# Kernel optimization log

Measured on AMD Instinct MI355X. Metric: run time of the kernel, lower is better.

Reference implementation:

```python
import jax, jax.numpy as jnp
import numpy as np

N = 2048
C = 1024
B = 4
LN_EPS = 1e-5
SCALE = 1.0 / np.sqrt(N)  # module uses 1/sqrt(n), not 1/sqrt(d)


def setup_inputs() -> dict:
    key = jax.random.key(0)
    ks = jax.random.split(key, 4)
    x = jax.random.normal(ks[0], (B, C, N), dtype=jnp.float32)
    position = jax.random.normal(ks[1], (N, N), dtype=jnp.float32)
    ln_gamma = jnp.ones((C,), dtype=jnp.float32)
    ln_beta = jnp.zeros((C,), dtype=jnp.float32)
    W_qkv = jax.random.normal(ks[2], (3 * C, C), dtype=jnp.float32) / np.sqrt(C)
    b_qkv = jnp.zeros((3 * C,), dtype=jnp.float32)
    return {"x": x, "position": position, "ln_gamma": ln_gamma,
            "ln_beta": ln_beta, "W_qkv": W_qkv, "b_qkv": b_qkv}


def reference(x, position, ln_gamma, ln_beta, W_qkv, b_qkv):
    # x: [B, C, N] -> tokens-last layout; permute to [B, N, C]
    h = jnp.transpose(x, (0, 2, 1))
    # LayerNorm over channel dim
    mu = jnp.mean(h, axis=-1, keepdims=True)
    var = jnp.mean(jnp.square(h - mu), axis=-1, keepdims=True)
    h = (h - mu) * jax.lax.rsqrt(var + LN_EPS) * ln_gamma + ln_beta
    # QKV projection: torch Linear -> h @ W^T + b
    qkv = jnp.einsum('bnc,dc->bnd', h, W_qkv) + b_qkv
    q, k, v = jnp.split(qkv, 3, axis=-1)  # each [B, N, C]
    # scores: [B, N, N] with learned additive position bias
    scores = jnp.einsum('bic,bjc->bij', q, k) * SCALE + position
    attn = jax.nn.softmax(scores, axis=-1)
    out = jnp.einsum('bij,bjc->bic', attn, v)  # [B, N, C]
    return jnp.transpose(out, (0, 2, 1))  # [B, C, N]
```

## Files before the change

### kernel.cpp

```cpp
#include <hip/hip_runtime.h>
#include <stdint.h>

typedef unsigned short u16;
typedef unsigned int u32;

#define NTOK 2048
#define CDIM 1024
#define BSZ  4
#define MTOT (BSZ * NTOK)
#define QKVD 3072
#define SM_SCALE 0.02209708691207961f
#define INV_SM_SCALE 45.254833995939045f

typedef __bf16 bf16x8 __attribute__((ext_vector_type(8)));
typedef float f32x4 __attribute__((ext_vector_type(4)));

__device__ __forceinline__ u16 f2bf(float f) {
  u32 u = __float_as_uint(f);
  u += 0x7fffu + ((u >> 16) & 1u);
  return (u16)(u >> 16);
}

__global__ __launch_bounds__(256) void wconv_kernel(const float* __restrict__ W,
                                                    u16* __restrict__ Wb, int n8,
                                                    float* __restrict__ RS) {
  int i = blockIdx.x * 256 + threadIdx.x;
  if (i < MTOT) RS[i] = 0.f;
  if (i >= n8) return;
  const float4* p = (const float4*)W + (size_t)i * 2;
  float4 a = p[0], b = p[1];
  uint4 o;
  o.x = (u32)f2bf(a.x) | ((u32)f2bf(a.y) << 16);
  o.y = (u32)f2bf(a.z) | ((u32)f2bf(a.w) << 16);
  o.z = (u32)f2bf(b.x) | ((u32)f2bf(b.y) << 16);
  o.w = (u32)f2bf(b.z) | ((u32)f2bf(b.w) << 16);
  ((uint4*)Wb)[i] = o;
}

__global__ __launch_bounds__(512) void ln_kernel(const float* __restrict__ x,
                                                 const float* __restrict__ gamma,
                                                 const float* __restrict__ beta,
                                                 u16* __restrict__ h) {
  int blk = blockIdx.x;
  int b = blk >> 6;
  int n0 = (blk & 63) << 5;
  int t = threadIdx.x;
  int nl = t & 31;
  int cp = t >> 5;
  const float* xb = x + (size_t)b * CDIM * NTOK + n0 + nl;

  float v[64];
  float s = 0.f, ss = 0.f;
#pragma unroll
  for (int k = 0; k < 64; ++k) {
    v[k] = xb[(size_t)(cp + (k << 4)) * NTOK];
    s += v[k]; ss += v[k] * v[k];
  }
  __shared__ float ps[16][32], pss[16][32];
  __shared__ float mean_s[32], rstd_s[32];
  ps[cp][nl] = s; pss[cp][nl] = ss;
  __syncthreads();
  if (t < 32) {
    float m = 0.f, q = 0.f;
#pragma unroll
    for (int p = 0; p < 16; ++p) { m += ps[p][t]; q += pss[p][t]; }
    float mu = m * (1.f / CDIM);
    float var = q * (1.f / CDIM) - mu * mu;
    mean_s[t] = mu;
    rstd_s[t] = rsqrtf(var + 1e-5f);
  }
  __syncthreads();
  float mu_n = mean_s[nl], rs_n = rstd_s[nl];

  __shared__ float tile[64][33];
  int tn = t >> 4, cl = t & 15;
#pragma unroll
  for (int kk = 0; kk < 16; ++kk) {
    __syncthreads();
#pragma unroll
    for (int i = 0; i < 4; ++i) {
      int c = (kk << 6) + (i << 4) + cp;
      tile[(i << 4) + cp][nl] = (v[(kk << 2) + i] - mu_n) * rs_n * gamma[c] + beta[c];
    }
    __syncthreads();
    uint2 pk;
    pk.x = (u32)f2bf(tile[(cl << 2) + 0][tn]) | ((u32)f2bf(tile[(cl << 2) + 1][tn]) << 16);
    pk.y = (u32)f2bf(tile[(cl << 2) + 2][tn]) | ((u32)f2bf(tile[(cl << 2) + 3][tn]) << 16);
    *(uint2*)&h[(size_t)(b * NTOK + n0 + tn) * CDIM + (kk << 6) + (cl << 2)] = pk;
  }
}

__device__ __forceinline__ void gld_lds16(const void* g, void* l) {
  __builtin_amdgcn_global_load_lds(
      (const __attribute__((address_space(1))) void*)g,
      (__attribute__((address_space(3))) void*)l, 16, 0, 0);
}

__device__ __forceinline__ void stage128(const char* g, long ld, char* lds, int t) {
  const long rb = (long)(t >> 2) * ld + ((((t & 3) - (t >> 3)) & 3) << 4);
#pragma unroll
  for (int i = 0; i < 2; ++i)
    gld_lds16(g + rb + (long)(i * 64) * ld,
              lds + ((t >> 6) << 10) + (i << 12));
}

template <int EPI>
__global__ __launch_bounds__(256, 3) void gemm_kernel(
    const u16* __restrict__ A, int lda, long sA,
    const u16* __restrict__ B, int ldb, long sB, int K,
    const float* __restrict__ bias,
    const float* __restrict__ pos,
    u16* __restrict__ Cb, int ldc, long sC,
    u16* __restrict__ KD,
    u16* __restrict__ VT,
    float* __restrict__ CT, long sCT,
    float* __restrict__ RS)
{
  __shared__ char smem[32768];

  const int GX = gridDim.x, GY = gridDim.y;
  const int hb = ((int)blockIdx.z * GY + blockIdx.y) * GX + blockIdx.x;
  const int MX = GX >> 3;
  const int k8 = hb & 7, j8 = hb >> 3;
  const int m = k8 * MX + (j8 % MX);
  const int rest = j8 / MX;
  const int n = rest % GY;
  const int bz = rest / GY;

  A += (size_t)bz * sA;
  B += (size_t)bz * sB;
  const int bm0 = m * 128;
  const int bn0 = n * 128;

  const int t = threadIdx.x;
  const int wave = t >> 6;
  const int wm = wave >> 1, wn = wave & 1;
  const int MROW = wm * 64, NCOL = wn * 64;
  const int lr = t & 15, lk = (t & 63) >> 4;
  const int fragoff = lr * 64 + (((lk + (lr >> 1)) & 3) << 4);

  const long lda2 = (long)lda * 2, ldb2 = (long)ldb * 2;
  const char* Agb = (const char*)A + (size_t)bm0 * lda2;
  const char* Bgb = (const char*)B + (size_t)bn0 * ldb2;

  f32x4 acc[4][4];
  if (EPI == 1) {
#pragma unroll
    for (int mm = 0; mm < 4; ++mm) {
      const int row = bm0 + MROW + mm * 16 + (lk << 2);
#pragma unroll
      for (int nn = 0; nn < 4; ++nn) {
        const int col = bn0 + NCOL + nn * 16 + lr;
#pragma unroll
        for (int r = 0; r < 4; ++r)
          acc[mm][nn][r] = pos[(size_t)(row + r) * NTOK + col] * INV_SM_SCALE;
      }
    }
  } else {
#pragma unroll
    for (int mm = 0; mm < 4; ++mm)
#pragma unroll
      for (int nn = 0; nn < 4; ++nn) acc[mm][nn] = (f32x4){0.f, 0.f, 0.f, 0.f};
  }

  const int nt = K >> 6;
  for (int kt = 0; kt < nt; ++kt) {
    __syncthreads();
    const long kb = (long)kt * 128;
    stage128(Agb + kb,      lda2, smem,          t);
    stage128(Agb + kb + 64, lda2, smem + 8192,   t);
    stage128(Bgb + kb,      ldb2, smem + 16384,  t);
    stage128(Bgb + kb + 64, ldb2, smem + 24576,  t);
    __syncthreads();

#pragma unroll
    for (int ks = 0; ks < 2; ++ks) {
      const char* Ab = smem + ks * 8192;
      const char* Bb = smem + 16384 + ks * 8192;
      bf16x8 av[4], bv[4];
#pragma unroll
      for (int i = 0; i < 4; ++i)
        av[i] = *(const bf16x8*)(Ab + (MROW + i * 16) * 64 + fragoff);
#pragma unroll
      for (int i = 0; i < 4; ++i)
        bv[i] = *(const bf16x8*)(Bb + (NCOL + i * 16) * 64 + fragoff);
#pragma unroll
      for (int mm = 0; mm < 4; ++mm)
#pragma unroll
        for (int nn = 0; nn < 4; ++nn)
          acc[mm][nn] = __builtin_amdgcn_mfma_f32_16x16x32_bf16(av[mm], bv[nn],
                                                                acc[mm][nn], 0, 0, 0);
    }
  }

#pragma unroll
  for (int mm = 0; mm < 4; ++mm) {
    const int row = bm0 + MROW + mm * 16 + (lk << 2);
    float rs[4] = {0.f, 0.f, 0.f, 0.f};
    float inv[4];
    if (EPI == 2) {
      const float4 rsv = *(const float4*)(RS + (size_t)bz * NTOK + row);
      inv[0] = 1.f / rsv.x; inv[1] = 1.f / rsv.y;
      inv[2] = 1.f / rsv.z; inv[3] = 1.f / rsv.w;
    }
#pragma unroll
    for (int nn = 0; nn < 4; ++nn) {
      const int col = bn0 + NCOL + nn * 16 + lr;
      f32x4 v = acc[mm][nn];
      if (EPI == 0) {
        const float bb = bias[col];
        if (col < CDIM) {
#pragma unroll
          for (int r = 0; r < 4; ++r)
            Cb[(size_t)(row + r) * CDIM + col] = f2bf(v[r] + bb);
        } else if (col < 2 * CDIM) {
          const int c1 = col - CDIM;
#pragma unroll
          for (int r = 0; r < 4; ++r)
            KD[(size_t)(row + r) * CDIM + c1] = f2bf(v[r] + bb);
        } else {
          const int bq = row >> 11;
          const int j = row & (NTOK - 1);
          const int c2 = col - 2 * CDIM;
          uint2 pk;
          pk.x = (u32)f2bf(v[0] + bb) | ((u32)f2bf(v[1] + bb) << 16);
          pk.y = (u32)f2bf(v[2] + bb) | ((u32)f2bf(v[3] + bb) << 16);
          *(uint2*)&VT[((size_t)bq * CDIM + c2) * NTOK + j] = pk;
        }
      } else if (EPI == 1) {
        u16* Cp = Cb + (size_t)bz * sC;
#pragma unroll
        for (int r = 0; r < 4; ++r) {
          float e = __expf(v[r] * SM_SCALE);
          rs[r] += e;
          Cp[(size_t)(row + r) * ldc + col] = f2bf(e);
        }
      } else {
        float* o = CT + (size_t)bz * sCT + (size_t)col * NTOK + row;
        f32x4 w;
        w[0] = v[0] * inv[0]; w[1] = v[1] * inv[1];
        w[2] = v[2] * inv[2]; w[3] = v[3] * inv[3];
        *(f32x4*)o = w;
      }
    }
    if (EPI == 1) {
#pragma unroll
      for (int r = 0; r < 4; ++r) {
#pragma unroll
        for (int mk = 1; mk <= 8; mk <<= 1)
          rs[r] += __shfl_xor(rs[r], mk, 64);
      }
      if (lr == 0) {
        float* rp = RS + (size_t)bz * NTOK + row;
        atomicAdd(rp + 0, rs[0]);
        atomicAdd(rp + 1, rs[1]);
        atomicAdd(rp + 2, rs[2]);
        atomicAdd(rp + 3, rs[3]);
      }
    }
  }
}

extern "C" void kernel_launch(void* const* d_in, const int* in_sizes, int n_in,
                              void* d_out, int out_size, void* d_ws, size_t ws_size,
                              hipStream_t stream) {
  const float* x     = (const float*)d_in[0];
  const float* pos   = (const float*)d_in[1];
  const float* gamma = (const float*)d_in[2];
  const float* beta  = (const float*)d_in[3];
  const float* W     = (const float*)d_in[4];
  const float* bias  = (const float*)d_in[5];
  float* out = (float*)d_out;
  char* ws = (char*)d_ws;

  u16* Wb  = (u16*)(ws);
  u16* h   = (u16*)(ws + (6ll << 20));
  u16* qd  = (u16*)(ws + (22ll << 20));
  u16* kd  = (u16*)(ws + (38ll << 20));
  u16* vT  = (u16*)(ws + (54ll << 20));
  u16* S   = (u16*)(ws + (70ll << 20));
  float* RS = (float*)(ws + (102ll << 20));

  wconv_kernel<<<dim3((QKVD * CDIM / 8 + 255) / 256), 256, 0, stream>>>(
      W, Wb, QKVD * CDIM / 8, RS);
  ln_kernel<<<dim3(BSZ * (NTOK / 32)), 512, 0, stream>>>(x, gamma, beta, h);

  gemm_kernel<0><<<dim3(MTOT / 128, QKVD / 128, 1), 256, 0, stream>>>(
      h, CDIM, 0, Wb, CDIM, 0, CDIM,
      bias, nullptr, qd, CDIM, 0, kd, vT, nullptr, 0, nullptr);

  gemm_kernel<1><<<dim3(NTOK / 128, NTOK / 128, BSZ), 256, 0, stream>>>(
      qd, CDIM, (long)NTOK * CDIM, kd, CDIM, (long)NTOK * CDIM, CDIM,
      nullptr, pos, S, NTOK, (long)NTOK * NTOK, nullptr, nullptr, nullptr, 0, RS);

  gemm_kernel<2><<<dim3(NTOK / 128, CDIM / 128, BSZ), 256, 0, stream>>>(
      S, NTOK, (long)NTOK * NTOK, vT, NTOK, (long)CDIM * NTOK, NTOK,
      nullptr, nullptr, nullptr, 0, 0, nullptr, nullptr, out, (long)CDIM * NTOK, RS);
}
```

Before: 177.6 us.

## Stage GEMM epilogue stores through LDS for coalesced 16-byte writes

The Q/K and exp-score epilogues now write bf16 results into a swizzled shared-memory tile and then emit coalesced 16-byte row stores, replacing the scattered 2-byte stores. The position bias is no longer preloaded into the accumulators; it is added in the epilogue instead, which frees registers, and launch bounds for the score kernel are raised to 4 blocks per CU. The trade-off is extra syncthreads per row group and possible LDS bank conflicts. The V-transpose and output paths are split into separate early-return branches.

```diff
diff --git a/kernel.cpp b/kernel.cpp
--- a/kernel.cpp
+++ b/kernel.cpp
@@ -10,7 +10,6 @@
 #define MTOT (BSZ * NTOK)
 #define QKVD 3072
 #define SM_SCALE 0.02209708691207961f
-#define INV_SM_SCALE 45.254833995939045f
 
 typedef __bf16 bf16x8 __attribute__((ext_vector_type(8)));
 typedef float f32x4 __attribute__((ext_vector_type(4)));
@@ -105,7 +104,7 @@
 }
 
 template <int EPI>
-__global__ __launch_bounds__(256, 3) void gemm_kernel(
+__global__ __launch_bounds__(256, (EPI == 1) ? 4 : 3) void gemm_kernel(
     const u16* __restrict__ A, int lda, long sA,
     const u16* __restrict__ B, int ldb, long sB, int K,
     const float* __restrict__ bias,
@@ -144,24 +143,10 @@
   const char* Bgb = (const char*)B + (size_t)bn0 * ldb2;
 
   f32x4 acc[4][4];
-  if (EPI == 1) {
-#pragma unroll
-    for (int mm = 0; mm < 4; ++mm) {
-      const int row = bm0 + MROW + mm * 16 + (lk << 2);
-#pragma unroll
-      for (int nn = 0; nn < 4; ++nn) {
-        const int col = bn0 + NCOL + nn * 16 + lr;
-#pragma unroll
-        for (int r = 0; r < 4; ++r)
-          acc[mm][nn][r] = pos[(size_t)(row + r) * NTOK + col] * INV_SM_SCALE;
-      }
-    }
-  } else {
-#pragma unroll
-    for (int mm = 0; mm < 4; ++mm)
-#pragma unroll
-      for (int nn = 0; nn < 4; ++nn) acc[mm][nn] = (f32x4){0.f, 0.f, 0.f, 0.f};
-  }
+#pragma unroll
+  for (int mm = 0; mm < 4; ++mm)
+#pragma unroll
+    for (int nn = 0; nn < 4; ++nn) acc[mm][nn] = (f32x4){0.f, 0.f, 0.f, 0.f};
 
   const int nt = K >> 6;
   for (int kt = 0; kt < nt; ++kt) {
@@ -193,54 +178,83 @@
     }
   }
 
-#pragma unroll
-  for (int mm = 0; mm < 4; ++mm) {
-    const int row = bm0 + MROW + mm * 16 + (lk << 2);
-    float rs[4] = {0.f, 0.f, 0.f, 0.f};
-    float inv[4];
-    if (EPI == 2) {
+  if (EPI == 2) {
+#pragma unroll
+    for (int mm = 0; mm < 4; ++mm) {
+      const int row = bm0 + MROW + mm * 16 + (lk << 2);
       const float4 rsv = *(const float4*)(RS + (size_t)bz * NTOK + row);
-      inv[0] = 1.f / rsv.x; inv[1] = 1.f / rsv.y;
-      inv[2] = 1.f / rsv.z; inv[3] = 1.f / rsv.w;
-    }
-#pragma unroll
-    for (int nn = 0; nn < 4; ++nn) {
-      const int col = bn0 + NCOL + nn * 16 + lr;
-      f32x4 v = acc[mm][nn];
-      if (EPI == 0) {
-        const float bb = bias[col];
-        if (col < CDIM) {
-#pragma unroll
-          for (int r = 0; r < 4; ++r)
-            Cb[(size_t)(row + r) * CDIM + col] = f2bf(v[r] + bb);
-        } else if (col < 2 * CDIM) {
-          const int c1 = col - CDIM;
-#pragma unroll
-          for (int r = 0; r < 4; ++r)
-            KD[(size_t)(row + r) * CDIM + c1] = f2bf(v[r] + bb);
-        } else {
-          const int bq = row >> 11;
-          const int j = row & (NTOK - 1);
-          const int c2 = col - 2 * CDIM;
-          uint2 pk;
-          pk.x = (u32)f2bf(v[0] + bb) | ((u32)f2bf(v[1] + bb) << 16);
-          pk.y = (u32)f2bf(v[2] + bb) | ((u32)f2bf(v[3] + bb) << 16);
-          *(uint2*)&VT[((size_t)bq * CDIM + c2) * NTOK + j] = pk;
-        }
-      } else if (EPI == 1) {
-        u16* Cp = Cb + (size_t)bz * sC;
-#pragma unroll
-        for (int r = 0; r < 4; ++r) {
-          float e = __expf(v[r] * SM_SCALE);
-          rs[r] += e;
-          Cp[(size_t)(row + r) * ldc + col] = f2bf(e);
-        }
-      } else {
+      float inv[4] = {1.f / rsv.x, 1.f / rsv.y, 1.f / rsv.z, 1.f / rsv.w};
+#pragma unroll
+      for (int nn = 0; nn < 4; ++nn) {
+        const int col = bn0 + NCOL + nn * 16 + lr;
+        f32x4 v = acc[mm][nn];
         float* o = CT + (size_t)bz * sCT + (size_t)col * NTOK + row;
         f32x4 w;
         w[0] = v[0] * inv[0]; w[1] = v[1] * inv[1];
         w[2] = v[2] * inv[2]; w[3] = v[3] * inv[3];
         *(f32x4*)o = w;
+      }
+    }
+    return;
+  }
+
+  if (EPI == 0 && bn0 >= 2 * CDIM) {
+#pragma unroll
+    for (int mm = 0; mm < 4; ++mm) {
+      const int row = bm0 + MROW + mm * 16 + (lk << 2);
+#pragma unroll
+      for (int nn = 0; nn < 4; ++nn) {
+        const int col = bn0 + NCOL + nn * 16 + lr;
+        const float bb = bias[col];
+        f32x4 v = acc[mm][nn];
+        const int bq = row >> 11;
+        const int j = row & (NTOK - 1);
+        const int c2 = col - 2 * CDIM;
+        uint2 pk;
+        pk.x = (u32)f2bf(v[0] + bb) | ((u32)f2bf(v[1] + bb) << 16);
+        pk.y = (u32)f2bf(v[2] + bb) | ((u32)f2bf(v[3] + bb) << 16);
+        *(uint2*)&VT[((size_t)bq * CDIM + c2) * NTOK + j] = pk;
+      }
+    }
+    return;
+  }
+
+  u16* tb = (u16*)smem;
+  u16* dst;
+  int ldd, colbase;
+  if (EPI == 0) {
+    if (bn0 < CDIM) { dst = Cb; colbase = bn0; }
+    else            { dst = KD; colbase = bn0 - CDIM; }
+    ldd = CDIM;
+  } else {
+    dst = Cb + (size_t)bz * sC; colbase = bn0; ldd = ldc;
+  }
+  float bb[4];
+#pragma unroll
+  for (int nn = 0; nn < 4; ++nn)
+    bb[nn] = (EPI == 0) ? bias[bn0 + NCOL + nn * 16 + lr] : 0.f;
+
+#pragma unroll
+  for (int mm = 0; mm < 4; ++mm) {
+    const int row = bm0 + MROW + mm * 16 + (lk << 2);
+    float rs[4] = {0.f, 0.f, 0.f, 0.f};
+    __syncthreads();
+#pragma unroll
+    for (int nn = 0; nn < 4; ++nn) {
+      const int coll = NCOL + nn * 16 + lr;
+      f32x4 v = acc[mm][nn];
+#pragma unroll
+      for (int r = 0; r < 4; ++r) {
+        u16 ov;
+        if (EPI == 0) {
+          ov = f2bf(v[r] + bb[nn]);
+        } else {
+          float sv = v[r] * SM_SCALE + pos[(size_t)(row + r) * NTOK + colbase + coll];
+          float e = __expf(sv);
+          rs[r] += e;
+          ov = f2bf(e);
+        }
+        tb[(wm * 16 + lk * 4 + r) * 128 + (coll ^ (lk << 3))] = ov;
       }
     }
     if (EPI == 1) {
@@ -257,6 +271,18 @@
         atomicAdd(rp + 2, rs[2]);
         atomicAdd(rp + 3, rs[3]);
       }
+    }
+    __syncthreads();
+#pragma unroll
+    for (int i = 0; i < 2; ++i) {
+      const int u = i * 256 + t;
+      const int rsl = u >> 4;
+      const int cc  = u & 15;
+      const int band = rsl >> 4, r16 = rsl & 15;
+      const int grow = bm0 + band * 64 + mm * 16 + r16;
+      const int ccs = cc ^ ((r16 >> 2) & 3);
+      *(uint4*)&dst[(size_t)grow * ldd + colbase + cc * 8] =
+          *(const uint4*)&tb[rsl * 128 + ccs * 8];
     }
   }
 }
```

Result: faster. 171.2 us (-3.6%).
